# Kernel tuning notes

Measured on AMD Instinct MI355X. Metric: run time of the kernel, lower is better.

## Reference

```python
import jax, jax.numpy as jnp
import numpy as np

B, S, DIM = 2, 2048, 2048
H, KVH, HD = 16, 4, 128
G = H // KVH  # GQA groups = 4
THETA = 10000.0


def setup_inputs() -> dict:
    key = jax.random.key(0)
    k0, k1, k2, k3, k4 = jax.random.split(key, 5)
    x = jax.random.normal(k0, (B, S, DIM), jnp.float32)
    # RoPE table: [max_seq_len, head_dim//2, 2] holding (cos, sin)
    inv_freq = 1.0 / (THETA ** (jnp.arange(0, HD, 2, dtype=jnp.float32) / HD))
    angles = jnp.outer(jnp.arange(S, dtype=jnp.float32), inv_freq)  # [S, HD//2]
    freqs_cis = jnp.stack([jnp.cos(angles), jnp.sin(angles)], axis=-1)
    sc = 0.02
    wq = jax.random.normal(k1, (H * HD, DIM), jnp.float32) * sc
    wk = jax.random.normal(k2, (KVH * HD, DIM), jnp.float32) * sc
    wv = jax.random.normal(k3, (KVH * HD, DIM), jnp.float32) * sc
    wo = jax.random.normal(k4, (DIM, H * HD), jnp.float32) * sc
    return {"x": x, "freqs_cis": freqs_cis, "wq": wq, "wk": wk, "wv": wv, "wo": wo}


def apply_rope(x, freqs_cis):
    # x: [B, S, h, HD]; freqs_cis: [max_S, HD//2, 2]
    s = x.shape[1]
    xr = x.astype(jnp.float32).reshape(*x.shape[:-1], -1, 2)  # [B,S,h,HD//2,2]
    cos = freqs_cis[:s, :, 0][None, :, None, :]  # [1,S,1,HD//2]
    sin = freqs_cis[:s, :, 1][None, :, None, :]
    x0, x1 = xr[..., 0], xr[..., 1]
    out = jnp.stack([x0 * cos - x1 * sin, x0 * sin + x1 * cos], axis=-1)
    return out.reshape(x.shape).astype(x.dtype)


def reference(x, freqs_cis, wq, wk, wv, wo):
    b, s, d = x.shape
    q = (x @ wq.T).reshape(b, s, H, HD)
    k = (x @ wk.T).reshape(b, s, KVH, HD)
    v = (x @ wv.T).reshape(b, s, KVH, HD)
    q = apply_rope(q, freqs_cis)
    k = apply_rope(k, freqs_cis)
    # GQA expand: repeat_interleave along head dim
    k = jnp.repeat(k, G, axis=2)  # [b,s,H,HD]
    v = jnp.repeat(v, G, axis=2)
    q = jnp.swapaxes(q, 1, 2)  # [b,H,s,HD]
    k = jnp.swapaxes(k, 1, 2)
    v = jnp.swapaxes(v, 1, 2)
    scale = 1.0 / jnp.sqrt(jnp.asarray(HD, dtype=q.dtype))
    scores = jnp.einsum('bhqd,bhkd->bhqk', q, k) * scale  # [b,H,s,s]
    causal = jnp.tril(jnp.ones((s, s), dtype=bool))
    scores = jnp.where(causal[None, None], scores, jnp.finfo(scores.dtype).min)
    probs = jax.nn.softmax(scores, axis=-1)
    attn = jnp.einsum('bhqk,bhkd->bhqd', probs, v)  # [b,H,s,HD]
    attn = jnp.swapaxes(attn, 1, 2).reshape(b, s, H * HD)
    return attn @ wo.T
```

## Files before the change

### kernel.cpp

```cpp
#include <hip/hip_runtime.h>
#include <stdint.h>

#define B_ 2
#define S_ 2048
#define DIM_ 2048
#define H_ 16
#define KVH_ 4
#define HD_ 128

typedef short short8 __attribute__((ext_vector_type(8)));
typedef float f4 __attribute__((ext_vector_type(4)));
typedef unsigned short u16;

#define KSCALE (0.08838834764831845f * 1.4426950408889634f)

__device__ __forceinline__ float bf2f(u16 u) {
    union { unsigned int i; float f; } c; c.i = ((unsigned int)u) << 16; return c.f;
}
__device__ __forceinline__ u16 f2bf(float f) {
    union { float f; unsigned int i; } c; c.f = f;
    return (u16)((c.i + 0x7fffu + ((c.i >> 16) & 1u)) >> 16);
}

#define GLDS16(gp, lp) \
    __builtin_amdgcn_global_load_lds((const __attribute__((address_space(1))) unsigned int*)(gp), \
                                     (__attribute__((address_space(3))) unsigned int*)(lp), 16, 0, 0)

__global__ void cast_all(const float* __restrict__ x,  const float* __restrict__ wq,
                         const float* __restrict__ wk, const float* __restrict__ wv,
                         const float* __restrict__ wo,
                         u16* __restrict__ xb, u16* __restrict__ wqkvb, u16* __restrict__ wob) {
    int i = blockIdx.x * 256 + threadIdx.x;
    const float4* src; ushort4* dst; int j;
    if (i < 2097152)      { src = (const float4*)x;  dst = (ushort4*)xb;                 j = i; }
    else if (i < 3145728) { src = (const float4*)wq; dst = (ushort4*)wqkvb;              j = i - 2097152; }
    else if (i < 3407872) { src = (const float4*)wk; dst = (ushort4*)wqkvb + 1048576;    j = i - 3145728; }
    else if (i < 3670016) { src = (const float4*)wv; dst = (ushort4*)wqkvb + 1310720;    j = i - 3407872; }
    else                  { src = (const float4*)wo; dst = (ushort4*)wob;                j = i - 3670016; }
    float4 v = src[j];
    ushort4 o;
    o.x = f2bf(v.x); o.y = f2bf(v.y); o.z = f2bf(v.z); o.w = f2bf(v.w);
    dst[j] = o;
}

template<bool OUT_BF16>
__global__ __launch_bounds__(256) void gemm_bt(const u16* __restrict__ A,
                                               const u16* __restrict__ W,
                                               void* __restrict__ Cout,
                                               int M, int N, int K) {
    __shared__ u16 As[128 * 32];
    __shared__ u16 Bs[128 * 32];
    int t = threadIdx.x, lane = t & 63, w = t >> 6;
    int quad = lane >> 4, l16 = lane & 15;
    int wm = w & 1, wn = w >> 1;
    size_t m0 = (size_t)blockIdx.y * 128, n0 = (size_t)blockIdx.x * 128;

    int c0 = w * 2;
    int ar = c0 * 16 + (lane >> 2);
    int ac = (lane & 3) * 8;
    const u16* Abase = A + (m0 + ar) * (size_t)K + ac;
    const u16* Bbase = W + (n0 + ar) * (size_t)K + ac;
    u16* Adst = As + c0 * 512;
    u16* Bdst = Bs + c0 * 512;

    f4 acc[4][4];
    #pragma unroll
    for (int i = 0; i < 4; i++)
        #pragma unroll
        for (int j = 0; j < 4; j++) acc[i][j] = (f4){0.f, 0.f, 0.f, 0.f};

    int nk = K >> 5;
    for (int kt = 0; kt < nk; kt++) {
        const u16* ga = Abase + kt * 32;
        const u16* gb = Bbase + kt * 32;
        GLDS16(ga, Adst);
        GLDS16(ga + 16 * (size_t)K, Adst + 512);
        GLDS16(gb, Bdst);
        GLDS16(gb + 16 * (size_t)K, Bdst + 512);
        __syncthreads();
        short8 a[4], b[4];
        #pragma unroll
        for (int i = 0; i < 4; i++) a[i] = *(const short8*)&As[(wm * 64 + i * 16 + l16) * 32 + quad * 8];
        #pragma unroll
        for (int j = 0; j < 4; j++) b[j] = *(const short8*)&Bs[(wn * 64 + j * 16 + l16) * 32 + quad * 8];
        #pragma unroll
        for (int i = 0; i < 4; i++)
            #pragma unroll
            for (int j = 0; j < 4; j++)
                acc[i][j] = __builtin_amdgcn_mfma_f32_16x16x32_bf16(a[i], b[j], acc[i][j], 0, 0, 0);
        __syncthreads();
    }
    #pragma unroll
    for (int i = 0; i < 4; i++) {
        size_t row = m0 + wm * 64 + i * 16 + quad * 4;
        #pragma unroll
        for (int j = 0; j < 4; j++) {
            size_t col = n0 + wn * 64 + j * 16 + l16;
            #pragma unroll
            for (int r = 0; r < 4; r++) {
                if (OUT_BF16) ((u16*)Cout)[(row + r) * N + col] = f2bf(acc[i][j][r]);
                else          ((float*)Cout)[(row + r) * N + col] = acc[i][j][r];
            }
        }
    }
}

__global__ void rope_q(u16* __restrict__ QKV, const float* __restrict__ freqs) {
    int pc = blockIdx.x * 256 + threadIdx.x;
    int row = blockIdx.y;
    int s = row & (S_ - 1);
    int hd2 = pc & 63;
    float2 cs = ((const float2*)freqs)[s * 64 + hd2];
    ushort2* pp = (ushort2*)(QKV + (size_t)row * 3072);
    ushort2 v = pp[pc];
    float x0 = bf2f(v.x), x1 = bf2f(v.y);
    ushort2 ov;
    ov.x = f2bf((x0 * cs.x - x1 * cs.y) * KSCALE);
    ov.y = f2bf((x0 * cs.y + x1 * cs.x) * KSCALE);
    pp[pc] = ov;
}

__global__ __launch_bounds__(256) void pack_k(const u16* __restrict__ QKV,
                                              const float* __restrict__ freqs,
                                              u16* __restrict__ Kp) {
    int gid = blockIdx.x * 256 + threadIdx.x;
    int lane = gid & 63;
    int fid = (gid >> 6) & 15;
    int kt = (gid >> 10) & 31;
    int bk = gid >> 15;
    int b = bk >> 2, kvh = bk & 3;
    int n = fid >> 2, c = fid & 3;
    int l16 = lane & 15, quad = lane >> 4;
    int s = kt * 64 + n * 16 + l16;
    const u16* src = QKV + (size_t)(b * 2048 + s) * 3072 + 2048 + kvh * 128 + c * 32 + quad * 8;
    short8 v = *(const short8*)src;
    short8 o;
    #pragma unroll
    for (int jp = 0; jp < 4; jp++) {
        int hd2 = c * 16 + quad * 4 + jp;
        float2 cw = ((const float2*)freqs)[s * 64 + hd2];
        float x0 = bf2f((u16)v[2 * jp]), x1 = bf2f((u16)v[2 * jp + 1]);
        o[2 * jp]     = (short)f2bf(x0 * cw.x - x1 * cw.y);
        o[2 * jp + 1] = (short)f2bf(x0 * cw.y + x1 * cw.x);
    }
    *(short8*)&Kp[(size_t)gid * 8] = o;
}

__global__ __launch_bounds__(256) void pack_v(const u16* __restrict__ QKV, u16* __restrict__ Vp) {
    __shared__ u16 L[64 * 136];
    int bid = blockIdx.x;
    int bk = bid & 7, kt = bid >> 3;
    int b = bk >> 2, kvh = bk & 3;
    int t = threadIdx.x;
    const u16* src = QKV + (size_t)(b * 2048 + kt * 64) * 3072 + 2560 + kvh * 128;
    #pragma unroll
    for (int it = 0; it < 4; it++) {
        int idx = t + it * 256;
        int r = idx >> 4, c = idx & 15;
        *(short8*)&L[r * 136 + c * 8] = *(const short8*)(src + (size_t)r * 3072 + c * 8);
    }
    __syncthreads();
    u16* dst = Vp + ((size_t)bk * 32 + kt) * 8192;
    #pragma unroll
    for (int it = 0; it < 4; it++) {
        int idx = t + it * 256;
        int fid = idx >> 6, lane = idx & 63;
        int nt = fid >> 1, kc = fid & 1;
        int l16 = lane & 15, quad = lane >> 4;
        int hd = nt * 16 + l16;
        int s0 = kc * 32 + quad * 8;
        short8 v;
        #pragma unroll
        for (int j = 0; j < 8; j++) v[j] = (short)L[(s0 + j) * 136 + hd];
        *(short8*)&dst[(size_t)idx * 8] = v;
    }
}

__global__ __launch_bounds__(256) __attribute__((amdgpu_waves_per_eu(2, 2)))
void attn_kernel(const u16* __restrict__ QKV,
                 const u16* __restrict__ Kp,
                 const u16* __restrict__ Vp,
                 u16* __restrict__ Ob) {
    __shared__ u16 Ks[16 * 512];
    __shared__ u16 Vs[16 * 512];
    __shared__ u16 Ps[4 * 1024];
    int bid = blockIdx.x;
    int bk = bid & 7, pr = bid >> 3;
    int b = bk >> 2, kvh = bk & 3;
    int t = threadIdx.x, lane = t & 63, w = t >> 6, quad = lane >> 4, l16 = lane & 15;
    int l7 = l16 & 7, hi = l16 >> 3;
    int h = kvh * 4 + w;

    short8 ones;
    #pragma unroll
    for (int j = 0; j < 8; j++) ones[j] = (short)0x3F80;

    const u16* Kpb = Kp + (size_t)bk * 32 * 8192;
    const u16* Vpb = Vp + (size_t)bk * 32 * 8192;
    u16* P = Ps + w * 1024;

    for (int ph = 0; ph < 2; ph++) {
        int qt = ph ? pr : 127 - pr;
        int nkt = (qt >> 2) + 1;

        short8 qf[4];
        {
            const u16* qp = QKV + ((size_t)(b * S_ + qt * 16 + l16)) * 3072 + h * HD_ + quad * 8;
            #pragma unroll
            for (int c = 0; c < 4; c++) qf[c] = *(const short8*)(qp + c * 32);
        }
        float m_i = -3e38f;
        f4 ls = (f4){0.f, 0.f, 0.f, 0.f};
        f4 o[8];
        #pragma unroll
        for (int n = 0; n < 8; n++) o[n] = (f4){0.f, 0.f, 0.f, 0.f};

        for (int kt = 0; kt < nkt; kt++) {
            {
                const u16* ks = Kpb + (size_t)kt * 8192 + (w * 4) * 512 + lane * 8;
                const u16* vs = Vpb + (size_t)kt * 8192 + (w * 4) * 512 + lane * 8;
                #pragma unroll
                for (int i = 0; i < 4; i++) {
                    GLDS16(ks + i * 512, &Ks[(w * 4 + i) * 512]);
                    GLDS16(vs + i * 512, &Vs[(w * 4 + i) * 512]);
                }
            }
            __syncthreads();

            f4 sc[4];
            #pragma unroll
            for (int n = 0; n < 4; n++) sc[n] = (f4){0.f, 0.f, 0.f, 0.f};
            #pragma unroll
            for (int n = 0; n < 4; n++) {
                #pragma unroll
                for (int c = 0; c < 4; c++) {
                    short8 kf = *(const short8*)&Ks[(n * 4 + c) * 512 + lane * 8];
                    sc[n] = __builtin_amdgcn_mfma_f32_16x16x32_bf16(qf[c], kf, sc[n], 0, 0, 0);
                }
            }
            if (kt == nkt - 1) {
                int qrow0 = qt * 16 + quad * 4;
                #pragma unroll
                for (int n = 0; n < 4; n++) {
                    int colg = kt * 64 + n * 16 + l16;
                    #pragma unroll
                    for (int r = 0; r < 4; r++)
                        sc[n][r] = (colg <= qrow0 + r) ? sc[n][r] : -3e38f;
                }
            }
            float gm = fmaxf(fmaxf(sc[0][0], sc[0][1]), fmaxf(sc[0][2], sc[0][3]));
            #pragma unroll
            for (int n = 1; n < 4; n++)
                gm = fmaxf(gm, fmaxf(fmaxf(sc[n][0], sc[n][1]), fmaxf(sc[n][2], sc[n][3])));
            #pragma unroll
            for (int off = 1; off < 64; off <<= 1) gm = fmaxf(gm, __shfl_xor(gm, off, 64));
            float mnew = fmaxf(m_i, gm);
            if (mnew > m_i) {
                float al = exp2f(m_i - mnew);
                m_i = mnew;
                #pragma unroll
                for (int r = 0; r < 4; r++) ls[r] *= al;
                #pragma unroll
                for (int nt = 0; nt < 8; nt++)
                    #pragma unroll
                    for (int r = 0; r < 4; r++) o[nt][r] *= al;
            }
            #pragma unroll
            for (int n = 0; n < 4; n++) {
                #pragma unroll
                for (int r = 0; r < 4; r++) {
                    float p = exp2f(sc[n][r] - m_i);
                    union { float f; unsigned int u; } cv; cv.f = p;
                    int row = quad * 4 + r;
                    int sw = (n * 2 + hi) ^ (row & 7);
                    P[row * 64 + sw * 8 + l7] = (u16)(cv.u >> 16);
                }
            }
            __asm__ volatile("s_waitcnt lgkmcnt(0)" ::: "memory");

            #pragma unroll
            for (int kc = 0; kc < 2; kc++) {
                short8 af = *(const short8*)&P[l16 * 64 + (((kc * 4 + quad) ^ l7) << 3)];
                ls = __builtin_amdgcn_mfma_f32_16x16x32_bf16(af, ones, ls, 0, 0, 0);
                #pragma unroll
                for (int nt = 0; nt < 8; nt++) {
                    short8 vf = *(const short8*)&Vs[(nt * 2 + kc) * 512 + lane * 8];
                    o[nt] = __builtin_amdgcn_mfma_f32_16x16x32_bf16(af, vf, o[nt], 0, 0, 0);
                }
            }
            __syncthreads();
        }
        float rl[4];
        #pragma unroll
        for (int r = 0; r < 4; r++) rl[r] = 1.0f / ls[r];
        #pragma unroll
        for (int nt = 0; nt < 8; nt++)
            #pragma unroll
            for (int r = 0; r < 4; r++) {
                size_t row = (size_t)b * S_ + qt * 16 + quad * 4 + r;
                Ob[row * 2048 + h * HD_ + nt * 16 + l16] = f2bf(o[nt][r] * rl[r]);
            }
    }
}

extern "C" void kernel_launch(void* const* d_in, const int* in_sizes, int n_in,
                              void* d_out, int out_size, void* d_ws, size_t ws_size,
                              hipStream_t stream) {
    const float* x     = (const float*)d_in[0];
    const float* freqs = (const float*)d_in[1];
    const float* wq    = (const float*)d_in[2];
    const float* wk    = (const float*)d_in[3];
    const float* wv    = (const float*)d_in[4];
    const float* wo    = (const float*)d_in[5];
    float* out = (float*)d_out;

    char* p = (char*)d_ws;
    u16* xb    = (u16*)p; p += (size_t)4096 * 2048 * 2;
    u16* wqkvb = (u16*)p; p += (size_t)3072 * 2048 * 2;
    u16* wob   = (u16*)p; p += (size_t)2048 * 2048 * 2;
    u16* QKVb  = (u16*)p; p += (size_t)4096 * 3072 * 2;
    u16* Kpb   = (u16*)p; p += (size_t)8 * 32 * 8192 * 2;
    u16* Vpb   = (u16*)p; p += (size_t)8 * 32 * 8192 * 2;
    u16* attnb = xb;

    cast_all<<<18432, 256, 0, stream>>>(x, wq, wk, wv, wo, xb, wqkvb, wob);

    gemm_bt<true><<<dim3(24, 32), 256, 0, stream>>>(xb, wqkvb, QKVb, 4096, 3072, 2048);

    rope_q<<<dim3(4, 4096), 256, 0, stream>>>(QKVb, freqs);

    pack_k<<<1024, 256, 0, stream>>>(QKVb, freqs, Kpb);
    pack_v<<<256, 256, 0, stream>>>(QKVb, Vpb);

    attn_kernel<<<512, 256, 0, stream>>>(QKVb, Kpb, Vpb, attnb);

    gemm_bt<false><<<dim3(16, 32), 256, 0, stream>>>(attnb, wob, out, 4096, 2048, 2048);
}
```

Before: 324.0 us.

## Fuse Q RoPE into attention, rebalance attention work split, XCD-aware GEMM tiling

Removes the separate rope_q kernel and applies RoPE plus the softmax scale to Q fragments as they are loaded inside the attention kernel. The attention grid doubles: each block now covers two heads, with waves 0-1 taking a long query tile and waves 2-3 a short one sharing K/V loads. Occupancy is raised to 4 waves per EU. The GEMMs use a 1D grid remapped so consecutive blocks on the same XCD share M rows for L2 reuse. The trade-off is that the short-tile waves sit idle through the remaining K/V steps, and the higher wave count puts more pressure on registers.

```diff
diff --git a/kernel.cpp b/kernel.cpp
--- a/kernel.cpp
+++ b/kernel.cpp
@@ -43,7 +43,7 @@
     dst[j] = o;
 }
 
-template<bool OUT_BF16>
+template<bool OUT_BF16, int NBX>
 __global__ __launch_bounds__(256) void gemm_bt(const u16* __restrict__ A,
                                                const u16* __restrict__ W,
                                                void* __restrict__ Cout,
@@ -53,7 +53,10 @@
     int t = threadIdx.x, lane = t & 63, w = t >> 6;
     int quad = lane >> 4, l16 = lane & 15;
     int wm = w & 1, wn = w >> 1;
-    size_t m0 = (size_t)blockIdx.y * 128, n0 = (size_t)blockIdx.x * 128;
+    int bid = blockIdx.x;
+    int xcd = bid & 7, grp = bid >> 3;
+    int bx = grp % NBX, by = (grp / NBX) * 8 + xcd;
+    size_t m0 = (size_t)by * 128, n0 = (size_t)bx * 128;
 
     int c0 = w * 2;
     int ar = c0 * 16 + (lane >> 2);
@@ -103,21 +106,6 @@
             }
         }
     }
-}
-
-__global__ void rope_q(u16* __restrict__ QKV, const float* __restrict__ freqs) {
-    int pc = blockIdx.x * 256 + threadIdx.x;
-    int row = blockIdx.y;
-    int s = row & (S_ - 1);
-    int hd2 = pc & 63;
-    float2 cs = ((const float2*)freqs)[s * 64 + hd2];
-    ushort2* pp = (ushort2*)(QKV + (size_t)row * 3072);
-    ushort2 v = pp[pc];
-    float x0 = bf2f(v.x), x1 = bf2f(v.y);
-    ushort2 ov;
-    ov.x = f2bf((x0 * cs.x - x1 * cs.y) * KSCALE);
-    ov.y = f2bf((x0 * cs.y + x1 * cs.x) * KSCALE);
-    pp[pc] = ov;
 }
 
 __global__ __launch_bounds__(256) void pack_k(const u16* __restrict__ QKV,
@@ -176,8 +164,9 @@
     }
 }
 
-__global__ __launch_bounds__(256) __attribute__((amdgpu_waves_per_eu(2, 2)))
+__global__ __launch_bounds__(256) __attribute__((amdgpu_waves_per_eu(4, 4)))
 void attn_kernel(const u16* __restrict__ QKV,
+                 const float* __restrict__ freqs,
                  const u16* __restrict__ Kp,
                  const u16* __restrict__ Vp,
                  u16* __restrict__ Ob) {
@@ -185,48 +174,61 @@
     __shared__ u16 Vs[16 * 512];
     __shared__ u16 Ps[4 * 1024];
     int bid = blockIdx.x;
-    int bk = bid & 7, pr = bid >> 3;
+    int bk = bid & 7, pr = (bid >> 3) & 63, half = bid >> 9;
     int b = bk >> 2, kvh = bk & 3;
     int t = threadIdx.x, lane = t & 63, w = t >> 6, quad = lane >> 4, l16 = lane & 15;
     int l7 = l16 & 7, hi = l16 >> 3;
-    int h = kvh * 4 + w;
+    int h = kvh * 4 + half * 2 + (w & 1);
+    int qt = (w < 2) ? (127 - pr) : pr;
+    int nkt = (qt >> 2) + 1;
+    int nktL = 32 - (pr >> 2);
 
     short8 ones;
     #pragma unroll
     for (int j = 0; j < 8; j++) ones[j] = (short)0x3F80;
+
+    short8 qf[4];
+    {
+        int s = qt * 16 + l16;
+        const u16* qp = QKV + ((size_t)(b * S_ + s)) * 3072 + h * HD_ + quad * 8;
+        const float2* fr2 = (const float2*)freqs;
+        #pragma unroll
+        for (int c = 0; c < 4; c++) {
+            short8 v = *(const short8*)(qp + c * 32);
+            short8 o;
+            #pragma unroll
+            for (int jp = 0; jp < 4; jp++) {
+                float2 cs = fr2[s * 64 + c * 16 + quad * 4 + jp];
+                float x0 = bf2f((u16)v[2 * jp]), x1 = bf2f((u16)v[2 * jp + 1]);
+                o[2 * jp]     = (short)f2bf((x0 * cs.x - x1 * cs.y) * KSCALE);
+                o[2 * jp + 1] = (short)f2bf((x0 * cs.y + x1 * cs.x) * KSCALE);
+            }
+            qf[c] = o;
+        }
+    }
+    float m_i = -3e38f;
+    f4 ls = (f4){0.f, 0.f, 0.f, 0.f};
+    f4 o[8];
+    #pragma unroll
+    for (int n = 0; n < 8; n++) o[n] = (f4){0.f, 0.f, 0.f, 0.f};
 
     const u16* Kpb = Kp + (size_t)bk * 32 * 8192;
     const u16* Vpb = Vp + (size_t)bk * 32 * 8192;
     u16* P = Ps + w * 1024;
 
-    for (int ph = 0; ph < 2; ph++) {
-        int qt = ph ? pr : 127 - pr;
-        int nkt = (qt >> 2) + 1;
-
-        short8 qf[4];
+    for (int kt = 0; kt < nktL; kt++) {
         {
-            const u16* qp = QKV + ((size_t)(b * S_ + qt * 16 + l16)) * 3072 + h * HD_ + quad * 8;
-            #pragma unroll
-            for (int c = 0; c < 4; c++) qf[c] = *(const short8*)(qp + c * 32);
-        }
-        float m_i = -3e38f;
-        f4 ls = (f4){0.f, 0.f, 0.f, 0.f};
-        f4 o[8];
-        #pragma unroll
-        for (int n = 0; n < 8; n++) o[n] = (f4){0.f, 0.f, 0.f, 0.f};
-
-        for (int kt = 0; kt < nkt; kt++) {
-            {
-                const u16* ks = Kpb + (size_t)kt * 8192 + (w * 4) * 512 + lane * 8;
-                const u16* vs = Vpb + (size_t)kt * 8192 + (w * 4) * 512 + lane * 8;
-                #pragma unroll
-                for (int i = 0; i < 4; i++) {
-                    GLDS16(ks + i * 512, &Ks[(w * 4 + i) * 512]);
-                    GLDS16(vs + i * 512, &Vs[(w * 4 + i) * 512]);
-                }
-            }
-            __syncthreads();
-
+            const u16* ks = Kpb + (size_t)kt * 8192 + (w * 4) * 512 + lane * 8;
+            const u16* vs = Vpb + (size_t)kt * 8192 + (w * 4) * 512 + lane * 8;
+            #pragma unroll
+            for (int i = 0; i < 4; i++) {
+                GLDS16(ks + i * 512, &Ks[(w * 4 + i) * 512]);
+                GLDS16(vs + i * 512, &Vs[(w * 4 + i) * 512]);
+            }
+        }
+        __syncthreads();
+
+        if (kt < nkt) {
             f4 sc[4];
             #pragma unroll
             for (int n = 0; n < 4; n++) sc[n] = (f4){0.f, 0.f, 0.f, 0.f};
@@ -288,19 +290,19 @@
                     o[nt] = __builtin_amdgcn_mfma_f32_16x16x32_bf16(af, vf, o[nt], 0, 0, 0);
                 }
             }
-            __syncthreads();
-        }
-        float rl[4];
-        #pragma unroll
-        for (int r = 0; r < 4; r++) rl[r] = 1.0f / ls[r];
-        #pragma unroll
-        for (int nt = 0; nt < 8; nt++)
-            #pragma unroll
-            for (int r = 0; r < 4; r++) {
-                size_t row = (size_t)b * S_ + qt * 16 + quad * 4 + r;
-                Ob[row * 2048 + h * HD_ + nt * 16 + l16] = f2bf(o[nt][r] * rl[r]);
-            }
-    }
+        }
+        __syncthreads();
+    }
+    float rl[4];
+    #pragma unroll
+    for (int r = 0; r < 4; r++) rl[r] = 1.0f / ls[r];
+    #pragma unroll
+    for (int nt = 0; nt < 8; nt++)
+        #pragma unroll
+        for (int r = 0; r < 4; r++) {
+            size_t row = (size_t)b * S_ + qt * 16 + quad * 4 + r;
+            Ob[row * 2048 + h * HD_ + nt * 16 + l16] = f2bf(o[nt][r] * rl[r]);
+        }
 }
 
 extern "C" void kernel_launch(void* const* d_in, const int* in_sizes, int n_in,
@@ -325,14 +327,12 @@
 
     cast_all<<<18432, 256, 0, stream>>>(x, wq, wk, wv, wo, xb, wqkvb, wob);
 
-    gemm_bt<true><<<dim3(24, 32), 256, 0, stream>>>(xb, wqkvb, QKVb, 4096, 3072, 2048);
-
-    rope_q<<<dim3(4, 4096), 256, 0, stream>>>(QKVb, freqs);
+    gemm_bt<true, 24><<<768, 256, 0, stream>>>(xb, wqkvb, QKVb, 4096, 3072, 2048);
 
     pack_k<<<1024, 256, 0, stream>>>(QKVb, freqs, Kpb);
     pack_v<<<256, 256, 0, stream>>>(QKVb, Vpb);
 
-    attn_kernel<<<512, 256, 0, stream>>>(QKVb, Kpb, Vpb, attnb);
-
-    gemm_bt<false><<<dim3(16, 32), 256, 0, stream>>>(attnb, wob, out, 4096, 2048, 2048);
-}
+    attn_kernel<<<1024, 256, 0, stream>>>(QKVb, freqs, Kpb, Vpb, attnb);
+
+    gemm_bt<false, 16><<<512, 256, 0, stream>>>(attnb, wob, out, 4096, 2048, 2048);
+}
```

Measured after the change: 326.4 us. About the same (+0.7%).
